# Kernel tuning notes

Measured on AMD Instinct MI355X. Metric: run time of the kernel, lower is better.

Reference implementation:

```python
import jax, jax.numpy as jnp
import numpy as np

N, E = 50000, 800000
H, C, K = 8, 16, 4
LAMBD = 1.0
DECAY = [float(np.log(LAMBD / (k + 1) + (1 + 1e-06))) for k in range(K + 1)]


def setup_inputs() -> dict:
    key = jax.random.key(0)
    ks = jax.random.split(key, 10)
    s = 0.05  # keep activations stable over K hops
    return {
        "x": jax.random.normal(ks[0], (N, 256), jnp.float32),
        "edge_index": jax.random.randint(ks[1], (2, E), 0, N, jnp.int64),
        "W0": jax.random.normal(ks[2], (256, 128), jnp.float32) * s,
        "b0": jnp.zeros((128,), jnp.float32),
        "W1": jax.random.normal(ks[3], (128, 128), jnp.float32) * s,
        "b1": jnp.zeros((128,), jnp.float32),
        "Wout": jax.random.normal(ks[4], (128, 40), jnp.float32) * s,
        "bout": jnp.zeros((40,), jnp.float32),
        "hop_att0": jax.random.normal(ks[5], (H, C), jnp.float32) * s,
        "hop_atts": jax.random.normal(ks[6], (K, H, 2 * C), jnp.float32) * s,
        "atts": jax.random.normal(ks[7], (K, H, C), jnp.float32) * s,
        "hop_biases": jnp.ones((K + 1, H), jnp.float32),
    }


def _aero_forward(x, edge_index, W0, b0, W1, b1, Wout, bout,
                  hop_att0, hop_atts, atts, hop_biases):
    n = x.shape[0]
    # add self loops (cached_edge_index is None in the torch module)
    loops = jnp.arange(n, dtype=edge_index.dtype)
    row = jnp.concatenate([edge_index[0], loops])  # source j
    col = jnp.concatenate([edge_index[1], loops])  # target i

    # hid_feat_init (dropout p=0 -> identity); num_layers=2
    h = x @ W0 + b0
    h = jax.nn.elu(h) @ W1 + b1
    h = h.reshape(n, H, C)

    # k = 0 hop attention
    g = jnp.einsum('hc,nhc->nh', hop_att0, jax.nn.elu(h)) + hop_biases[0]
    z = h * g[..., None]
    z_scale = z * DECAY[0]

    for k in range(1, K + 1):
        # edge attention: gather, elementwise, degree-normalize
        zi = z_scale[col]          # [E', H, C] target
        zj = z_scale[row]          # [E', H, C] source
        a = jnp.einsum('hc,ehc->eh', atts[k - 1], jax.nn.elu(zi + zj))
        a = jax.nn.softplus(a) + 1e-06                       # [E', H]
        deg = jax.ops.segment_sum(a, col, num_segments=n)    # [N, H]
        dinv = jnp.where(deg > 0, deg ** -0.5, 0.0)
        a = dinv[row] * a * dinv[col]
        # propagate: scatter-add weighted source features onto targets
        h = jax.ops.segment_sum(a[..., None] * h[row], col, num_segments=n)
        # hop attention on concat(h, z_scale)
        hz = jax.nn.elu(jnp.concatenate([h, z_scale], axis=-1))  # [N, H, 2C]
        g = jnp.einsum('hc,nhc->nh', hop_atts[k - 1], hz) + hop_biases[k]
        z = z + h * g[..., None]
        z_scale = z * DECAY[k]

    # node classifier
    z = jax.nn.elu(z.reshape(n, H * C))
    return z @ Wout + bout


def reference(x, edge_index, W0, b0, W1, b1, Wout, bout,
              hop_att0, hop_atts, atts, hop_biases):
    return _aero_forward(x, edge_index, W0, b0, W1, b1, Wout, bout,
                         hop_att0, hop_atts, atts, hop_biases)
```

## Files before the change

kernel.cpp:

```cpp
#include <hip/hip_runtime.h>
#include <hip/hip_fp16.h>
#include <math.h>

#define NH 8
#define NC 16
#define HC 128

typedef __attribute__((ext_vector_type(4))) _Float16 half4;

__device__ __forceinline__ float eluf(float x) { return x > 0.f ? x : __expf(x) - 1.f; }
__device__ __forceinline__ float splusf(float x) { return fmaxf(x, 0.f) + __logf(1.f + __expf(-fabsf(x))); }

__global__ void count_kernel(const int* __restrict__ ei, int* __restrict__ cnt, int E, int E2) {
    int e = blockIdx.x * blockDim.x + threadIdx.x;
    if (e >= E2) return;
    int col = (e < E) ? ei[E + e] : (e - E);
    atomicAdd(&cnt[col], 1);
}

__global__ void scan1_kernel(const int* __restrict__ counts, int* __restrict__ ptr,
                             int* __restrict__ partials, int n) {
    __shared__ int tmp[256];
    int t = threadIdx.x;
    int i = blockIdx.x * 256 + t;
    int v = (i < n) ? counts[i] : 0;
    tmp[t] = v;
    __syncthreads();
    for (int off = 1; off < 256; off <<= 1) {
        int add = (t >= off) ? tmp[t - off] : 0;
        __syncthreads();
        tmp[t] += add;
        __syncthreads();
    }
    if (i < n) ptr[i] = tmp[t] - v;
    if (t == 255) partials[blockIdx.x] = tmp[255];
}

__global__ void scan2_kernel(int* __restrict__ partials, int nb) {
    __shared__ int tmp[256];
    int t = threadIdx.x;
    int v = (t < nb) ? partials[t] : 0;
    tmp[t] = v;
    __syncthreads();
    for (int off = 1; off < 256; off <<= 1) {
        int add = (t >= off) ? tmp[t - off] : 0;
        __syncthreads();
        tmp[t] += add;
        __syncthreads();
    }
    if (t < nb) partials[t] = tmp[t] - v;
}

__global__ void scan3_kernel(int* __restrict__ ptr, const int* __restrict__ partials,
                             int n, int total) {
    int i = blockIdx.x * 256 + threadIdx.x;
    if (i < n) ptr[i] += partials[blockIdx.x];
    if (i == 0) ptr[n] = total;
}

__global__ void fill_kernel(const int* __restrict__ ei, const int* __restrict__ ptr,
                            int* __restrict__ cursor, int* __restrict__ src, int E, int E2) {
    int e = blockIdx.x * blockDim.x + threadIdx.x;
    if (e >= E2) return;
    int col, row;
    if (e < E) { row = ei[e]; col = ei[E + e]; }
    else       { row = e - E; col = e - E; }
    int pos = ptr[col] + atomicAdd(&cursor[col], 1);
    src[pos] = row;
}

template<int K, bool ELU_OUT, bool HOP0>
__global__ __launch_bounds__(256)
void mlp_gemm(const float* __restrict__ A, const float* __restrict__ W,
              const float* __restrict__ bias, float* __restrict__ out, int M,
              float* __restrict__ z_out, _Float16* __restrict__ h16_out,
              _Float16* __restrict__ z16_out,
              const float* __restrict__ att0, const float* __restrict__ hb0) {
    __shared__ float As[16 * 68];
    __shared__ float Ws[16 * 132];
    const int tid = threadIdx.x;
    const int m0 = blockIdx.x * 64;
    const int tm = tid >> 4;
    const int tn = tid & 15;
    float acc[4][8];
#pragma unroll
    for (int i = 0; i < 4; ++i)
#pragma unroll
        for (int j = 0; j < 8; ++j) acc[i][j] = 0.f;

    const int ra = tid >> 2;
    const int qa = (tid & 3) * 4;

    for (int k0 = 0; k0 < K; k0 += 16) {
        float4 a = make_float4(0.f, 0.f, 0.f, 0.f);
        int garow = m0 + ra;
        if (garow < M) a = *(const float4*)(A + (size_t)garow * K + k0 + qa);
        float wv[8];
#pragma unroll
        for (int t = 0; t < 8; ++t) {
            int idx = tid + t * 256;
            int r = idx >> 7, c = idx & 127;
            wv[t] = W[(size_t)(k0 + r) * 128 + c];
        }
        __syncthreads();
        As[(qa + 0) * 68 + ra] = a.x; As[(qa + 1) * 68 + ra] = a.y;
        As[(qa + 2) * 68 + ra] = a.z; As[(qa + 3) * 68 + ra] = a.w;
#pragma unroll
        for (int t = 0; t < 8; ++t) {
            int idx = tid + t * 256;
            int r = idx >> 7, c = idx & 127;
            Ws[r * 132 + c] = wv[t];
        }
        __syncthreads();
#pragma unroll
        for (int kk = 0; kk < 16; ++kk) {
            float ar[4], wr[8];
            *(float4*)&ar[0] = *(const float4*)&As[kk * 68 + tm * 4];
            *(float4*)&wr[0] = *(const float4*)&Ws[kk * 132 + tn * 4];
            *(float4*)&wr[4] = *(const float4*)&Ws[kk * 132 + 64 + tn * 4];
#pragma unroll
            for (int i = 0; i < 4; ++i)
#pragma unroll
                for (int j = 0; j < 8; ++j)
                    acc[i][j] = fmaf(ar[i], wr[j], acc[i][j]);
        }
    }
#pragma unroll
    for (int i = 0; i < 4; ++i) {
        int r = m0 + tm * 4 + i;
        float vv[8];
#pragma unroll
        for (int c = 0; c < 2; ++c)
#pragma unroll
            for (int j = 0; j < 4; ++j) {
                float v = acc[i][c * 4 + j] + bias[c * 64 + tn * 4 + j];
                if (ELU_OUT) v = eluf(v);
                vv[c * 4 + j] = v;
            }
        if (HOP0) {
            float part[2];
#pragma unroll
            for (int c = 0; c < 2; ++c) {
                float p = 0.f;
#pragma unroll
                for (int j = 0; j < 4; ++j)
                    p += att0[c * 64 + tn * 4 + j] * eluf(vv[c * 4 + j]);
                p += __shfl_xor(p, 1);
                p += __shfl_xor(p, 2);
                part[c] = p;
            }
            if (r < M) {
#pragma unroll
                for (int c = 0; c < 2; ++c) {
                    float g = part[c] + hb0[4 * c + (tn >> 2)];
                    int coff = c * 64 + tn * 4;
                    _Float16* hp  = h16_out + ((size_t)r << 7) + coff;
                    _Float16* zhp = z16_out + ((size_t)r << 7) + coff;
                    float*    zp  = z_out   + ((size_t)r << 7) + coff;
                    half4 ho, zo;
                    float zz[4];
#pragma unroll
                    for (int j = 0; j < 4; ++j) zz[j] = vv[c * 4 + j] * g;
                    ho.x = (_Float16)vv[c * 4 + 0]; ho.y = (_Float16)vv[c * 4 + 1];
                    ho.z = (_Float16)vv[c * 4 + 2]; ho.w = (_Float16)vv[c * 4 + 3];
                    zo.x = (_Float16)zz[0]; zo.y = (_Float16)zz[1];
                    zo.z = (_Float16)zz[2]; zo.w = (_Float16)zz[3];
                    *(half4*)hp = ho;
                    *(half4*)zhp = zo;
                    *(float4*)zp = make_float4(zz[0], zz[1], zz[2], zz[3]);
                }
            }
        } else {
            if (r < M) {
#pragma unroll
                for (int c = 0; c < 2; ++c) {
                    float* op = out + (size_t)r * 128 + c * 64 + tn * 4;
                    *(float4*)op = make_float4(vv[c * 4 + 0], vv[c * 4 + 1],
                                               vv[c * 4 + 2], vv[c * 4 + 3]);
                }
            }
        }
    }
}

__global__ __launch_bounds__(256)
void passA_kernel(const _Float16* __restrict__ z16, const int* __restrict__ ptr,
                  const int* __restrict__ src, const float* __restrict__ att,
                  float decay, _Float16* __restrict__ a_e, float* __restrict__ dinv, int n) {
    int wid = (int)((blockIdx.x * 256u + threadIdx.x) >> 6);
    if (wid >= n) return;
    const int lane = threadIdx.x & 63;
    const int half = lane >> 5;
    const int q    = lane & 31;
    const int hd   = q >> 2;
    const unsigned i = (unsigned)wid;

    const half4 ziH = *(const half4*)(z16 + (i << 7) + (q << 2));
    float4 zi;
    zi.x = (float)ziH.x * decay; zi.y = (float)ziH.y * decay;
    zi.z = (float)ziH.z * decay; zi.w = (float)ziH.w * decay;
    const float4 av = *(const float4*)(att + (q << 2));

    int s0 = ptr[wid], s1 = ptr[wid + 1];
    float dacc = 0.f;
    int s = s0 + half;
    for (; s + 6 < s1; s += 8) {
        unsigned j0 = (unsigned)src[s];
        unsigned j1 = (unsigned)src[s + 2];
        unsigned j2 = (unsigned)src[s + 4];
        unsigned j3 = (unsigned)src[s + 6];
        const half4 r0 = *(const half4*)(z16 + (j0 << 7) + (q << 2));
        const half4 r1 = *(const half4*)(z16 + (j1 << 7) + (q << 2));
        const half4 r2 = *(const half4*)(z16 + (j2 << 7) + (q << 2));
        const half4 r3 = *(const half4*)(z16 + (j3 << 7) + (q << 2));
        float p0, p1, p2, p3;
        p0  = av.x * eluf(fmaf((float)r0.x, decay, zi.x));
        p0 += av.y * eluf(fmaf((float)r0.y, decay, zi.y));
        p0 += av.z * eluf(fmaf((float)r0.z, decay, zi.z));
        p0 += av.w * eluf(fmaf((float)r0.w, decay, zi.w));
        p1  = av.x * eluf(fmaf((float)r1.x, decay, zi.x));
        p1 += av.y * eluf(fmaf((float)r1.y, decay, zi.y));
        p1 += av.z * eluf(fmaf((float)r1.z, decay, zi.z));
        p1 += av.w * eluf(fmaf((float)r1.w, decay, zi.w));
        p2  = av.x * eluf(fmaf((float)r2.x, decay, zi.x));
        p2 += av.y * eluf(fmaf((float)r2.y, decay, zi.y));
        p2 += av.z * eluf(fmaf((float)r2.z, decay, zi.z));
        p2 += av.w * eluf(fmaf((float)r2.w, decay, zi.w));
        p3  = av.x * eluf(fmaf((float)r3.x, decay, zi.x));
        p3 += av.y * eluf(fmaf((float)r3.y, decay, zi.y));
        p3 += av.z * eluf(fmaf((float)r3.z, decay, zi.z));
        p3 += av.w * eluf(fmaf((float)r3.w, decay, zi.w));
        p0 += __shfl_xor(p0, 1); p1 += __shfl_xor(p1, 1);
        p2 += __shfl_xor(p2, 1); p3 += __shfl_xor(p3, 1);
        p0 += __shfl_xor(p0, 2); p1 += __shfl_xor(p1, 2);
        p2 += __shfl_xor(p2, 2); p3 += __shfl_xor(p3, 2);
        if ((q & 3) == 0) {
            float a0 = splusf(p0) + 1e-6f;
            float a1 = splusf(p1) + 1e-6f;
            float a2 = splusf(p2) + 1e-6f;
            float a3 = splusf(p3) + 1e-6f;
            a_e[((unsigned)s << 3) + hd] = (_Float16)a0;
            a_e[((unsigned)(s + 2) << 3) + hd] = (_Float16)a1;
            a_e[((unsigned)(s + 4) << 3) + hd] = (_Float16)a2;
            a_e[((unsigned)(s + 6) << 3) + hd] = (_Float16)a3;
            dacc += (a0 + a1) + (a2 + a3);
        }
    }
    for (; s < s1; s += 2) {
        unsigned j = (unsigned)src[s];
        const half4 r = *(const half4*)(z16 + (j << 7) + (q << 2));
        float p;
        p  = av.x * eluf(fmaf((float)r.x, decay, zi.x));
        p += av.y * eluf(fmaf((float)r.y, decay, zi.y));
        p += av.z * eluf(fmaf((float)r.z, decay, zi.z));
        p += av.w * eluf(fmaf((float)r.w, decay, zi.w));
        p += __shfl_xor(p, 1);
        p += __shfl_xor(p, 2);
        if ((q & 3) == 0) {
            float aval = splusf(p) + 1e-6f;
            a_e[((unsigned)s << 3) + hd] = (_Float16)aval;
            dacc += aval;
        }
    }
    dacc += __shfl_xor(dacc, 32);
    if (half == 0 && (q & 3) == 0) {
        dinv[(i << 3) + hd] = (dacc > 0.f) ? (1.f / sqrtf(dacc)) : 0.f;
    }
}

__global__ __launch_bounds__(256)
void passB_kernel(const _Float16* __restrict__ h_in, float* __restrict__ z,
                  _Float16* __restrict__ z16,
                  const int* __restrict__ ptr, const int* __restrict__ src,
                  const _Float16* __restrict__ a_e, const float* __restrict__ dinv,
                  const float* __restrict__ hatt, const float* __restrict__ hb,
                  float decay, _Float16* __restrict__ h_out, int n, int store_h) {
    int wid = (int)((blockIdx.x * 256u + threadIdx.x) >> 6);
    if (wid >= n) return;
    const int lane = threadIdx.x & 63;
    const int half = lane >> 5;
    const int q    = lane & 31;
    const int hd   = q >> 2;
    const unsigned i = (unsigned)wid;

    const float di = dinv[(i << 3) + hd];
    int s0 = ptr[wid], s1 = ptr[wid + 1];
    float ax = 0.f, ay = 0.f, az = 0.f, aw = 0.f;
    int s = s0 + half;
    for (; s + 6 < s1; s += 8) {
        unsigned j0 = (unsigned)src[s];
        unsigned j1 = (unsigned)src[s + 2];
        unsigned j2 = (unsigned)src[s + 4];
        unsigned j3 = (unsigned)src[s + 6];
        float w0 = (float)a_e[((unsigned)s << 3) + hd]       * dinv[(j0 << 3) + hd];
        float w1 = (float)a_e[((unsigned)(s + 2) << 3) + hd] * dinv[(j1 << 3) + hd];
        float w2 = (float)a_e[((unsigned)(s + 4) << 3) + hd] * dinv[(j2 << 3) + hd];
        float w3 = (float)a_e[((unsigned)(s + 6) << 3) + hd] * dinv[(j3 << 3) + hd];
        const half4 f0 = *(const half4*)(h_in + (j0 << 7) + (q << 2));
        const half4 f1 = *(const half4*)(h_in + (j1 << 7) + (q << 2));
        const half4 f2 = *(const half4*)(h_in + (j2 << 7) + (q << 2));
        const half4 f3 = *(const half4*)(h_in + (j3 << 7) + (q << 2));
        ax = fmaf(w0, (float)f0.x, ax); ay = fmaf(w0, (float)f0.y, ay);
        az = fmaf(w0, (float)f0.z, az); aw = fmaf(w0, (float)f0.w, aw);
        ax = fmaf(w1, (float)f1.x, ax); ay = fmaf(w1, (float)f1.y, ay);
        az = fmaf(w1, (float)f1.z, az); aw = fmaf(w1, (float)f1.w, aw);
        ax = fmaf(w2, (float)f2.x, ax); ay = fmaf(w2, (float)f2.y, ay);
        az = fmaf(w2, (float)f2.z, az); aw = fmaf(w2, (float)f2.w, aw);
        ax = fmaf(w3, (float)f3.x, ax); ay = fmaf(w3, (float)f3.y, ay);
        az = fmaf(w3, (float)f3.z, az); aw = fmaf(w3, (float)f3.w, aw);
    }
    for (; s < s1; s += 2) {
        unsigned j = (unsigned)src[s];
        float w = (float)a_e[((unsigned)s << 3) + hd] * dinv[(j << 3) + hd];
        const half4 f = *(const half4*)(h_in + (j << 7) + (q << 2));
        ax = fmaf(w, (float)f.x, ax); ay = fmaf(w, (float)f.y, ay);
        az = fmaf(w, (float)f.z, az); aw = fmaf(w, (float)f.w, aw);
    }
    ax += __shfl_xor(ax, 32);
    ay += __shfl_xor(ay, 32);
    az += __shfl_xor(az, 32);
    aw += __shfl_xor(aw, 32);

    const float4 hn = make_float4(di * ax, di * ay, di * az, di * aw);
    const float4 zv = *(const float4*)(z + (i << 7) + (q << 2));
    const float* hA = hatt + hd * 32 + ((q & 3) << 2);
    float p;
    p  = hA[0] * eluf(hn.x) + hA[1] * eluf(hn.y)
       + hA[2] * eluf(hn.z) + hA[3] * eluf(hn.w);
    p += hA[16] * eluf(zv.x * decay) + hA[17] * eluf(zv.y * decay)
       + hA[18] * eluf(zv.z * decay) + hA[19] * eluf(zv.w * decay);
    p += __shfl_xor(p, 1);
    p += __shfl_xor(p, 2);
    const float g = p + hb[hd];
    if (half == 0) {
        float4 zn = make_float4(zv.x + hn.x * g, zv.y + hn.y * g,
                                zv.z + hn.z * g, zv.w + hn.w * g);
        if (store_h) {
            half4 ho, zo;
            ho.x = (_Float16)hn.x; ho.y = (_Float16)hn.y;
            ho.z = (_Float16)hn.z; ho.w = (_Float16)hn.w;
            *(half4*)(h_out + (i << 7) + (q << 2)) = ho;
            zo.x = (_Float16)zn.x; zo.y = (_Float16)zn.y;
            zo.z = (_Float16)zn.z; zo.w = (_Float16)zn.w;
            *(half4*)(z16 + (i << 7) + (q << 2)) = zo;
        }
        *(float4*)(z + (i << 7) + (q << 2)) = zn;
    }
}

__global__ __launch_bounds__(256)
void gout_kernel(const float* __restrict__ z, const float* __restrict__ W,
                 const float* __restrict__ bias, float* __restrict__ out, int M) {
    __shared__ float zs[128 * 65];
    __shared__ float ws[128 * 40];
    const int tid = threadIdx.x;
    const int r0 = blockIdx.x * 64;
    for (int idx = tid; idx < 128 * 40; idx += 256) ws[idx] = W[idx];
    const int r = tid >> 2;
    const int q = tid & 3;
    {
        int grow = r0 + r;
#pragma unroll
        for (int t = 0; t < 8; ++t) {
            int k = q * 4 + t * 16;
            float4 v = make_float4(0.f, 0.f, 0.f, 0.f);
            if (grow < M) v = *(const float4*)(z + (size_t)grow * HC + k);
            zs[(k + 0) * 65 + r] = eluf(v.x);
            zs[(k + 1) * 65 + r] = eluf(v.y);
            zs[(k + 2) * 65 + r] = eluf(v.z);
            zs[(k + 3) * 65 + r] = eluf(v.w);
        }
    }
    __syncthreads();
    float acc[10];
#pragma unroll
    for (int j = 0; j < 10; ++j) acc[j] = bias[q * 10 + j];
    for (int k = 0; k < 128; ++k) {
        float zk = zs[k * 65 + r];
#pragma unroll
        for (int j = 0; j < 10; ++j)
            acc[j] = fmaf(zk, ws[k * 40 + q * 10 + j], acc[j]);
    }
    int grow = r0 + r;
    if (grow < M) {
        float* op = out + (size_t)grow * 40 + q * 10;
#pragma unroll
        for (int j = 0; j < 10; ++j) op[j] = acc[j];
    }
}

extern "C" void kernel_launch(void* const* d_in, const int* in_sizes, int n_in,
                              void* d_out, int out_size, void* d_ws, size_t ws_size,
                              hipStream_t stream) {
    (void)n_in; (void)out_size; (void)ws_size;
    const float* x    = (const float*)d_in[0];
    const int*   ei   = (const int*)d_in[1];
    const float* W0   = (const float*)d_in[2];
    const float* b0   = (const float*)d_in[3];
    const float* W1   = (const float*)d_in[4];
    const float* b1   = (const float*)d_in[5];
    const float* Wout = (const float*)d_in[6];
    const float* bout = (const float*)d_in[7];
    const float* att0 = (const float*)d_in[8];
    const float* hatts= (const float*)d_in[9];
    const float* atts = (const float*)d_in[10];
    const float* hb   = (const float*)d_in[11];
    float* out = (float*)d_out;

    const int N  = in_sizes[0] / 256;
    const int E  = in_sizes[1] / 2;
    const int E2 = E + N;

    char* p = (char*)d_ws;
    auto carve = [&](size_t bytes) -> char* {
        char* r = p;
        p += (bytes + 255) & ~(size_t)255;
        return r;
    };
    float*    h1     = (float*)carve((size_t)N * HC * 4);
    _Float16* hbufA  = (_Float16*)carve((size_t)N * HC * 2);
    _Float16* hbufB  = (_Float16*)carve((size_t)N * HC * 2);
    float*    zbuf   = (float*)carve((size_t)N * HC * 4);
    _Float16* z16buf = (_Float16*)carve((size_t)N * HC * 2);
    _Float16* a_e    = (_Float16*)carve((size_t)E2 * NH * 2);
    float*    dinvb  = (float*)carve((size_t)N * NH * 4);
    int* csr_ptr   = (int*)carve((size_t)(N + 1) * 4);
    int* csr_src   = (int*)carve((size_t)E2 * 4);
    int* cursor    = (int*)carve((size_t)N * 4);
    int* partials  = (int*)carve(1024 * 4);

    float decay[5];
    for (int k = 0; k <= 4; ++k) decay[k] = (float)log(1.0 / (k + 1) + 1.0 + 1e-6);

    hipMemsetAsync(cursor, 0, (size_t)N * 4, stream);
    int eb = (E2 + 255) / 256;
    int nb = (N + 255) / 256;
    count_kernel<<<eb, 256, 0, stream>>>(ei, cursor, E, E2);
    scan1_kernel<<<nb, 256, 0, stream>>>(cursor, csr_ptr, partials, N);
    scan2_kernel<<<1, 256, 0, stream>>>(partials, nb);
    scan3_kernel<<<nb, 256, 0, stream>>>(csr_ptr, partials, N, E2);
    hipMemsetAsync(cursor, 0, (size_t)N * 4, stream);
    fill_kernel<<<eb, 256, 0, stream>>>(ei, csr_ptr, cursor, csr_src, E, E2);

    int gb = (N + 63) / 64;
    mlp_gemm<256, true , false><<<gb, 256, 0, stream>>>(x,  W0, b0, h1, N,
                                                        nullptr, nullptr, nullptr,
                                                        nullptr, nullptr);
    mlp_gemm<128, false, true ><<<gb, 256, 0, stream>>>(h1, W1, b1, nullptr, N,
                                                        zbuf, hbufA, z16buf, att0, hb);

    _Float16* hin  = hbufA;
    _Float16* hout = hbufB;
    int wb = (N + 3) / 4;
    for (int k = 1; k <= 4; ++k) {
        passA_kernel<<<wb, 256, 0, stream>>>(z16buf, csr_ptr, csr_src,
                                             atts + (size_t)(k - 1) * NH * NC,
                                             decay[k - 1], a_e, dinvb, N);
        passB_kernel<<<wb, 256, 0, stream>>>(hin, zbuf, z16buf, csr_ptr, csr_src,
                                             a_e, dinvb,
                                             hatts + (size_t)(k - 1) * NH * 32,
                                             hb + (size_t)k * NH, decay[k - 1], hout, N,
                                             (k < 4) ? 1 : 0);
        _Float16* t = hin; hin = hout; hout = t;
    }

    gout_kernel<<<(N + 63) / 64, 256, 0, stream>>>(zbuf, Wout, bout, out, N);
}
```

Baseline: 717.4 us.

## Process four edges per wavefront with 16-byte gathers and cheaper ELU math

The per-node edge attention and propagation kernels now split each 64-lane wavefront into four groups of 16 lanes. Each lane loads 8 half values (16 bytes) instead of 4, so four edges are in flight per step instead of two. The attention pass also rewrites the ELU-weighted dot product algebraically: the sum of exp2 terms and positive parts is accumulated, and the constant sum of attention weights is subtracted once. This removes per-element selects and the minus-one terms. The changes aim to cut memory instructions and ALU work in the gather-bound passes, at the cost of more registers and wider cross-group reductions.

```diff
diff --git a/kernel.cpp b/kernel.cpp
--- a/kernel.cpp
+++ b/kernel.cpp
@@ -7,9 +7,16 @@
 #define HC 128
 
 typedef __attribute__((ext_vector_type(4))) _Float16 half4;
+typedef __attribute__((ext_vector_type(8))) _Float16 half8;
 
 __device__ __forceinline__ float eluf(float x) { return x > 0.f ? x : __expf(x) - 1.f; }
 __device__ __forceinline__ float splusf(float x) { return fmaxf(x, 0.f) + __logf(1.f + __expf(-fabsf(x))); }
+
+#if __has_builtin(__builtin_amdgcn_exp2f)
+#define EXP2F(x) __builtin_amdgcn_exp2f(x)
+#else
+#define EXP2F(x) exp2f(x)
+#endif
 
 __global__ void count_kernel(const int* __restrict__ ei, int* __restrict__ cnt, int E, int E2) {
     int e = blockIdx.x * blockDim.x + threadIdx.x;
@@ -190,81 +197,76 @@
     int wid = (int)((blockIdx.x * 256u + threadIdx.x) >> 6);
     if (wid >= n) return;
     const int lane = threadIdx.x & 63;
-    const int half = lane >> 5;
-    const int q    = lane & 31;
-    const int hd   = q >> 2;
+    const int g  = lane >> 4;
+    const int q  = lane & 15;
+    const int hd = q >> 1;
     const unsigned i = (unsigned)wid;
-
-    const half4 ziH = *(const half4*)(z16 + (i << 7) + (q << 2));
-    float4 zi;
-    zi.x = (float)ziH.x * decay; zi.y = (float)ziH.y * decay;
-    zi.z = (float)ziH.z * decay; zi.w = (float)ziH.w * decay;
-    const float4 av = *(const float4*)(att + (q << 2));
-
-    int s0 = ptr[wid], s1 = ptr[wid + 1];
+    const float dl2 = decay * 1.44269504089f;
+
+    float ziL[8];
+    {
+        const half8 zi = *(const half8*)(z16 + ((size_t)i << 7) + (q << 3));
+#pragma unroll
+        for (int c = 0; c < 8; ++c) ziL[c] = (float)zi[c] * dl2;
+    }
+    float av[8];
+    *(float4*)&av[0] = *(const float4*)(att + (q << 3));
+    *(float4*)&av[4] = *(const float4*)(att + (q << 3) + 4);
+    float sav = ((av[0] + av[1]) + (av[2] + av[3]))
+              + ((av[4] + av[5]) + (av[6] + av[7]));
+    sav += __shfl_xor(sav, 1);
+
+    const int s0 = ptr[wid], s1 = ptr[wid + 1];
     float dacc = 0.f;
-    int s = s0 + half;
-    for (; s + 6 < s1; s += 8) {
-        unsigned j0 = (unsigned)src[s];
-        unsigned j1 = (unsigned)src[s + 2];
-        unsigned j2 = (unsigned)src[s + 4];
-        unsigned j3 = (unsigned)src[s + 6];
-        const half4 r0 = *(const half4*)(z16 + (j0 << 7) + (q << 2));
-        const half4 r1 = *(const half4*)(z16 + (j1 << 7) + (q << 2));
-        const half4 r2 = *(const half4*)(z16 + (j2 << 7) + (q << 2));
-        const half4 r3 = *(const half4*)(z16 + (j3 << 7) + (q << 2));
-        float p0, p1, p2, p3;
-        p0  = av.x * eluf(fmaf((float)r0.x, decay, zi.x));
-        p0 += av.y * eluf(fmaf((float)r0.y, decay, zi.y));
-        p0 += av.z * eluf(fmaf((float)r0.z, decay, zi.z));
-        p0 += av.w * eluf(fmaf((float)r0.w, decay, zi.w));
-        p1  = av.x * eluf(fmaf((float)r1.x, decay, zi.x));
-        p1 += av.y * eluf(fmaf((float)r1.y, decay, zi.y));
-        p1 += av.z * eluf(fmaf((float)r1.z, decay, zi.z));
-        p1 += av.w * eluf(fmaf((float)r1.w, decay, zi.w));
-        p2  = av.x * eluf(fmaf((float)r2.x, decay, zi.x));
-        p2 += av.y * eluf(fmaf((float)r2.y, decay, zi.y));
-        p2 += av.z * eluf(fmaf((float)r2.z, decay, zi.z));
-        p2 += av.w * eluf(fmaf((float)r2.w, decay, zi.w));
-        p3  = av.x * eluf(fmaf((float)r3.x, decay, zi.x));
-        p3 += av.y * eluf(fmaf((float)r3.y, decay, zi.y));
-        p3 += av.z * eluf(fmaf((float)r3.z, decay, zi.z));
-        p3 += av.w * eluf(fmaf((float)r3.w, decay, zi.w));
-        p0 += __shfl_xor(p0, 1); p1 += __shfl_xor(p1, 1);
-        p2 += __shfl_xor(p2, 1); p3 += __shfl_xor(p3, 1);
-        p0 += __shfl_xor(p0, 2); p1 += __shfl_xor(p1, 2);
-        p2 += __shfl_xor(p2, 2); p3 += __shfl_xor(p3, 2);
-        if ((q & 3) == 0) {
-            float a0 = splusf(p0) + 1e-6f;
-            float a1 = splusf(p1) + 1e-6f;
-            float a2 = splusf(p2) + 1e-6f;
-            float a3 = splusf(p3) + 1e-6f;
-            a_e[((unsigned)s << 3) + hd] = (_Float16)a0;
-            a_e[((unsigned)(s + 2) << 3) + hd] = (_Float16)a1;
-            a_e[((unsigned)(s + 4) << 3) + hd] = (_Float16)a2;
-            a_e[((unsigned)(s + 6) << 3) + hd] = (_Float16)a3;
-            dacc += (a0 + a1) + (a2 + a3);
-        }
-    }
-    for (; s < s1; s += 2) {
-        unsigned j = (unsigned)src[s];
-        const half4 r = *(const half4*)(z16 + (j << 7) + (q << 2));
-        float p;
-        p  = av.x * eluf(fmaf((float)r.x, decay, zi.x));
-        p += av.y * eluf(fmaf((float)r.y, decay, zi.y));
-        p += av.z * eluf(fmaf((float)r.z, decay, zi.z));
-        p += av.w * eluf(fmaf((float)r.w, decay, zi.w));
-        p += __shfl_xor(p, 1);
-        p += __shfl_xor(p, 2);
-        if ((q & 3) == 0) {
-            float aval = splusf(p) + 1e-6f;
-            a_e[((unsigned)s << 3) + hd] = (_Float16)aval;
-            dacc += aval;
-        }
-    }
+
+#define PA_BODY(f, sv) do {                                                  \
+        float pm = 0.f, pe = 0.f;                                            \
+        _Pragma("unroll")                                                    \
+        for (int c = 0; c < 8; ++c) {                                        \
+            float y = fmaf((float)(f)[c], dl2, ziL[c]);                      \
+            float e2 = EXP2F(fminf(y, 0.f));                                 \
+            pm = fmaf(av[c], fmaxf(y, 0.f), pm);                             \
+            pe = fmaf(av[c], e2, pe);                                        \
+        }                                                                    \
+        float pc = fmaf(pm, 0.69314718056f, pe);                             \
+        pc += __shfl_xor(pc, 1);                                             \
+        if ((q & 1) == 0) {                                                  \
+            float aval = splusf(pc - sav) + 1e-6f;                           \
+            a_e[((size_t)(sv) << 3) + hd] = (_Float16)aval;                  \
+            dacc += aval;                                                    \
+        }                                                                    \
+    } while (0)
+
+    const int nfull = (s1 - s0) & ~7;
+    const int send = s0 + nfull;
+    for (int s = s0 + g; s < send; s += 8) {
+        unsigned ja = (unsigned)src[s];
+        unsigned jb = (unsigned)src[s + 4];
+        const half8 fa = *(const half8*)(z16 + ((size_t)ja << 7) + (q << 3));
+        const half8 fb = *(const half8*)(z16 + ((size_t)jb << 7) + (q << 3));
+        PA_BODY(fa, s);
+        PA_BODY(fb, s + 4);
+    }
+    {
+        int sA = send + g;
+        if (sA < s1) {
+            unsigned ja = (unsigned)src[sA];
+            const half8 fa = *(const half8*)(z16 + ((size_t)ja << 7) + (q << 3));
+            PA_BODY(fa, sA);
+        }
+        int sB = send + 4 + g;
+        if (sB < s1) {
+            unsigned jb = (unsigned)src[sB];
+            const half8 fb = *(const half8*)(z16 + ((size_t)jb << 7) + (q << 3));
+            PA_BODY(fb, sB);
+        }
+    }
+#undef PA_BODY
+
+    dacc += __shfl_xor(dacc, 16);
     dacc += __shfl_xor(dacc, 32);
-    if (half == 0 && (q & 3) == 0) {
-        dinv[(i << 3) + hd] = (dacc > 0.f) ? (1.f / sqrtf(dacc)) : 0.f;
+    if ((lane & 0x31) == 0) {
+        dinv[((size_t)i << 3) + hd] = (dacc > 0.f) ? (1.f / sqrtf(dacc)) : 0.f;
     }
 }
 
@@ -278,73 +280,90 @@
     int wid = (int)((blockIdx.x * 256u + threadIdx.x) >> 6);
     if (wid >= n) return;
     const int lane = threadIdx.x & 63;
-    const int half = lane >> 5;
-    const int q    = lane & 31;
-    const int hd   = q >> 2;
+    const int g  = lane >> 4;
+    const int q  = lane & 15;
+    const int hd = q >> 1;
     const unsigned i = (unsigned)wid;
 
-    const float di = dinv[(i << 3) + hd];
-    int s0 = ptr[wid], s1 = ptr[wid + 1];
-    float ax = 0.f, ay = 0.f, az = 0.f, aw = 0.f;
-    int s = s0 + half;
-    for (; s + 6 < s1; s += 8) {
-        unsigned j0 = (unsigned)src[s];
-        unsigned j1 = (unsigned)src[s + 2];
-        unsigned j2 = (unsigned)src[s + 4];
-        unsigned j3 = (unsigned)src[s + 6];
-        float w0 = (float)a_e[((unsigned)s << 3) + hd]       * dinv[(j0 << 3) + hd];
-        float w1 = (float)a_e[((unsigned)(s + 2) << 3) + hd] * dinv[(j1 << 3) + hd];
-        float w2 = (float)a_e[((unsigned)(s + 4) << 3) + hd] * dinv[(j2 << 3) + hd];
-        float w3 = (float)a_e[((unsigned)(s + 6) << 3) + hd] * dinv[(j3 << 3) + hd];
-        const half4 f0 = *(const half4*)(h_in + (j0 << 7) + (q << 2));
-        const half4 f1 = *(const half4*)(h_in + (j1 << 7) + (q << 2));
-        const half4 f2 = *(const half4*)(h_in + (j2 << 7) + (q << 2));
-        const half4 f3 = *(const half4*)(h_in + (j3 << 7) + (q << 2));
-        ax = fmaf(w0, (float)f0.x, ax); ay = fmaf(w0, (float)f0.y, ay);
-        az = fmaf(w0, (float)f0.z, az); aw = fmaf(w0, (float)f0.w, aw);
-        ax = fmaf(w1, (float)f1.x, ax); ay = fmaf(w1, (float)f1.y, ay);
-        az = fmaf(w1, (float)f1.z, az); aw = fmaf(w1, (float)f1.w, aw);
-        ax = fmaf(w2, (float)f2.x, ax); ay = fmaf(w2, (float)f2.y, ay);
-        az = fmaf(w2, (float)f2.z, az); aw = fmaf(w2, (float)f2.w, aw);
-        ax = fmaf(w3, (float)f3.x, ax); ay = fmaf(w3, (float)f3.y, ay);
-        az = fmaf(w3, (float)f3.z, az); aw = fmaf(w3, (float)f3.w, aw);
-    }
-    for (; s < s1; s += 2) {
-        unsigned j = (unsigned)src[s];
-        float w = (float)a_e[((unsigned)s << 3) + hd] * dinv[(j << 3) + hd];
-        const half4 f = *(const half4*)(h_in + (j << 7) + (q << 2));
-        ax = fmaf(w, (float)f.x, ax); ay = fmaf(w, (float)f.y, ay);
-        az = fmaf(w, (float)f.z, az); aw = fmaf(w, (float)f.w, aw);
-    }
-    ax += __shfl_xor(ax, 32);
-    ay += __shfl_xor(ay, 32);
-    az += __shfl_xor(az, 32);
-    aw += __shfl_xor(aw, 32);
-
-    const float4 hn = make_float4(di * ax, di * ay, di * az, di * aw);
-    const float4 zv = *(const float4*)(z + (i << 7) + (q << 2));
-    const float* hA = hatt + hd * 32 + ((q & 3) << 2);
-    float p;
-    p  = hA[0] * eluf(hn.x) + hA[1] * eluf(hn.y)
-       + hA[2] * eluf(hn.z) + hA[3] * eluf(hn.w);
-    p += hA[16] * eluf(zv.x * decay) + hA[17] * eluf(zv.y * decay)
-       + hA[18] * eluf(zv.z * decay) + hA[19] * eluf(zv.w * decay);
+    const float di = dinv[((size_t)i << 3) + hd];
+    const int s0 = ptr[wid], s1 = ptr[wid + 1];
+    float acc[8];
+#pragma unroll
+    for (int c = 0; c < 8; ++c) acc[c] = 0.f;
+
+    const int nfull = (s1 - s0) & ~7;
+    const int send = s0 + nfull;
+    for (int s = s0 + g; s < send; s += 8) {
+        unsigned ja = (unsigned)src[s];
+        unsigned jb = (unsigned)src[s + 4];
+        const _Float16 aA = a_e[((size_t)s << 3) + hd];
+        const _Float16 aB = a_e[((size_t)(s + 4) << 3) + hd];
+        const float dA = dinv[((size_t)ja << 3) + hd];
+        const float dB = dinv[((size_t)jb << 3) + hd];
+        const half8 fa = *(const half8*)(h_in + ((size_t)ja << 7) + (q << 3));
+        const half8 fb = *(const half8*)(h_in + ((size_t)jb << 7) + (q << 3));
+        const float wa = (float)aA * dA;
+        const float wb = (float)aB * dB;
+#pragma unroll
+        for (int c = 0; c < 8; ++c) acc[c] = fmaf((float)fa[c], wa, acc[c]);
+#pragma unroll
+        for (int c = 0; c < 8; ++c) acc[c] = fmaf((float)fb[c], wb, acc[c]);
+    }
+    {
+        int sA = send + g;
+        if (sA < s1) {
+            unsigned j = (unsigned)src[sA];
+            const float w = (float)a_e[((size_t)sA << 3) + hd] * dinv[((size_t)j << 3) + hd];
+            const half8 f = *(const half8*)(h_in + ((size_t)j << 7) + (q << 3));
+#pragma unroll
+            for (int c = 0; c < 8; ++c) acc[c] = fmaf((float)f[c], w, acc[c]);
+        }
+        int sB = send + 4 + g;
+        if (sB < s1) {
+            unsigned j = (unsigned)src[sB];
+            const float w = (float)a_e[((size_t)sB << 3) + hd] * dinv[((size_t)j << 3) + hd];
+            const half8 f = *(const half8*)(h_in + ((size_t)j << 7) + (q << 3));
+#pragma unroll
+            for (int c = 0; c < 8; ++c) acc[c] = fmaf((float)f[c], w, acc[c]);
+        }
+    }
+#pragma unroll
+    for (int c = 0; c < 8; ++c) {
+        acc[c] += __shfl_xor(acc[c], 16);
+        acc[c] += __shfl_xor(acc[c], 32);
+    }
+
+    float hn[8];
+#pragma unroll
+    for (int c = 0; c < 8; ++c) hn[c] = di * acc[c];
+
+    float* zrow = z + ((size_t)i << 7) + (q << 3);
+    const float4 zva = *(const float4*)zrow;
+    const float4 zvb = *(const float4*)(zrow + 4);
+    float zv[8] = {zva.x, zva.y, zva.z, zva.w, zvb.x, zvb.y, zvb.z, zvb.w};
+
+    const float* hA = hatt + hd * 32 + (q & 1) * 8;
+    float p = 0.f;
+#pragma unroll
+    for (int c = 0; c < 8; ++c) p = fmaf(hA[c], eluf(hn[c]), p);
+#pragma unroll
+    for (int c = 0; c < 8; ++c) p = fmaf(hA[16 + c], eluf(zv[c] * decay), p);
     p += __shfl_xor(p, 1);
-    p += __shfl_xor(p, 2);
-    const float g = p + hb[hd];
-    if (half == 0) {
-        float4 zn = make_float4(zv.x + hn.x * g, zv.y + hn.y * g,
-                                zv.z + hn.z * g, zv.w + hn.w * g);
+    const float gv = p + hb[hd];
+
+    if (g == 0) {
+        float zn[8];
+#pragma unroll
+        for (int c = 0; c < 8; ++c) zn[c] = fmaf(hn[c], gv, zv[c]);
+        *(float4*)zrow       = make_float4(zn[0], zn[1], zn[2], zn[3]);
+        *(float4*)(zrow + 4) = make_float4(zn[4], zn[5], zn[6], zn[7]);
         if (store_h) {
-            half4 ho, zo;
-            ho.x = (_Float16)hn.x; ho.y = (_Float16)hn.y;
-            ho.z = (_Float16)hn.z; ho.w = (_Float16)hn.w;
-            *(half4*)(h_out + (i << 7) + (q << 2)) = ho;
-            zo.x = (_Float16)zn.x; zo.y = (_Float16)zn.y;
-            zo.z = (_Float16)zn.z; zo.w = (_Float16)zn.w;
-            *(half4*)(z16 + (i << 7) + (q << 2)) = zo;
-        }
-        *(float4*)(z + (i << 7) + (q << 2)) = zn;
+            half8 ho, zo;
+#pragma unroll
+            for (int c = 0; c < 8; ++c) { ho[c] = (_Float16)hn[c]; zo[c] = (_Float16)zn[c]; }
+            *(half8*)(h_out + ((size_t)i << 7) + (q << 3)) = ho;
+            *(half8*)(z16   + ((size_t)i << 7) + (q << 3)) = zo;
+        }
     }
 }
 
```

Result: faster. 671.9 us (-6.3%).
